# Kernel tuning notes

Measured on AMD Instinct MI355X. Metric: run time of the kernel, lower is better.

The kernel has to match this reference:

```python
import jax, jax.numpy as jnp
import numpy as np
import math

B, T, D, H, V, L = 8, 512, 128, 512, 50257, 8
DT = 1.0
RAW_INIT = math.log(math.expm1(1.0))  # so softplus(raw) == 1.0


def setup_inputs() -> dict:
    key = jax.random.key(0)
    ks = jax.random.split(key, 8)
    x = jax.random.randint(ks[0], (B, T), 0, V)
    E = jax.random.normal(ks[1], (V, D), jnp.float32) * 0.02
    P = jax.random.normal(ks[2], (T, D), jnp.float32) * 0.01
    W0 = jax.random.normal(ks[3], (2 * D, H), jnp.float32) * 0.02
    W1 = jax.random.normal(ks[4], (H, H), jnp.float32) * 0.02
    W2 = jax.random.normal(ks[5], (H, H), jnp.float32) * 0.02
    W3 = jax.random.normal(ks[6], (H, 1), jnp.float32) * 0.002
    return {
        'x': x, 'E': E, 'P': P,
        'W0': W0, 'b0': jnp.zeros((H,), jnp.float32),
        'W1': W1, 'b1': jnp.zeros((H,), jnp.float32),
        'W2': W2, 'b2': jnp.zeros((H,), jnp.float32),
        'W3': W3, 'b3': jnp.zeros((1,), jnp.float32),
        'raw_m_bias': jnp.asarray(RAW_INIT, jnp.float32),
        'raw_gamma': jnp.asarray(RAW_INIT, jnp.float32),
    }


def causal_cumulative_mean(h):
    t = h.shape[1]
    denom = jnp.arange(1, t + 1, dtype=h.dtype)[None, :, None]
    return jnp.cumsum(h, axis=1) / denom


def mlp_energy_sum(xi, h, W0, b0, W1, b1, W2, b2, W3, b3):
    z = jnp.concatenate([xi, h], axis=-1)  # (B,T,2D)
    z = jax.nn.gelu(z @ W0 + b0, approximate=False)
    z = jax.nn.gelu(z @ W1 + b1, approximate=False)
    z = jax.nn.gelu(z @ W2 + b2, approximate=False)
    return jnp.sum(z @ W3 + b3)


def reference(x, E, P, W0, b0, W1, b1, W2, b2, W3, b3, raw_m_bias, raw_gamma):
    emb = E[x] + P[None, :T]  # (B,T,D)
    gamma = jax.nn.softplus(raw_gamma)
    m = jax.nn.softplus(raw_m_bias) + 0.001  # global mass
    h = emb
    v = jnp.zeros_like(h)
    for _ in range(L):
        # causal_force=True: xi built from detached h
        xi = causal_cumulative_mean(jax.lax.stop_gradient(h))
        grad_V = jax.grad(
            lambda hh: mlp_energy_sum(xi, hh, W0, b0, W1, b1, W2, b2, W3, b3)
        )(h)
        f = -grad_V
        v = (v + DT * f / m) / (1.0 + DT * gamma)
        h = h + DT * v
    logits = jnp.einsum('btd,vd->btv', h, E)  # (B,T,V)
    return logits
```

## Files before the change

kernel.cpp:

```cpp
#include <hip/hip_runtime.h>
#include <hip/hip_bf16.h>

typedef __attribute__((ext_vector_type(8))) short short8;
typedef __attribute__((ext_vector_type(4))) float f32x4;

#define DEV static __device__ __forceinline__

DEV void gelu_pair(float x, float& z, float& dz){
  float ax = fabsf(x)*0.70710678118654752f;
  float e  = __expf(-ax*ax);
  float t  = __fdividef(1.0f, 1.0f + 0.3275911f*ax);
  float poly = t*(0.254829592f + t*(-0.284496736f + t*(1.421413741f +
               t*(-1.453152027f + t*1.061405429f))));
  float erfv = 1.0f - poly*e;
  erfv = x < 0.0f ? -erfv : erfv;
  float cdf = 0.5f*(1.0f + erfv);
  z  = x*cdf;
  dz = cdf + x*0.39894228040143268f*e;
}
DEV float dgelu_f(float x){ float zz, dz; gelu_pair(x, zz, dz); return dz; }
DEV float softplus_f(float x){ return log1pf(expf(x)); }
DEV void store_f4_a4(float* p, f32x4 v){ __builtin_memcpy(p, &v, 16); }

DEV void gload_lds16(const __hip_bfloat16* g, __hip_bfloat16* l){
  __builtin_amdgcn_global_load_lds((const __attribute__((address_space(1))) void*)g,
                                   (__attribute__((address_space(3))) void*)l, 16, 0, 0);
}

DEV unsigned pack2bf(float a, float b){
  __hip_bfloat16 ba = __float2bfloat16(a), bb = __float2bfloat16(b);
  unsigned short ua, ub;
  __builtin_memcpy(&ua, &ba, 2); __builtin_memcpy(&ub, &bb, 2);
  return (unsigned)ua | ((unsigned)ub << 16);
}
DEV float unp_lo(unsigned u){ union{unsigned x; float f;} c; c.x = u << 16; return c.f; }
DEV float unp_hi(unsigned u){ union{unsigned x; float f;} c; c.x = u & 0xffff0000u; return c.f; }

__global__ __launch_bounds__(512) void embed_k(const int* __restrict__ x,
                        const float* __restrict__ E, const float* __restrict__ P,
                        float* __restrict__ h, float* __restrict__ v,
                        float* __restrict__ S){
  int bid = blockIdx.x;
  int row = threadIdx.x >> 5;
  int q   = threadIdx.x & 31;
  int tok = bid*16 + row;
  int t   = tok & 511;
  int id  = x[tok];
  float4 e4 = ((const float4*)E)[(size_t)id*32 + q];
  float4 p4 = ((const float4*)P)[(size_t)t*32 + q];
  float4 val; val.x=e4.x+p4.x; val.y=e4.y+p4.y; val.z=e4.z+p4.z; val.w=e4.w+p4.w;
  float4 z4 = {0.f,0.f,0.f,0.f};
  ((float4*)h)[(size_t)tok*32 + q] = val;
  ((float4*)v)[(size_t)tok*32 + q] = z4;
  __shared__ float4 ps[16][32];
  ps[row][q] = val;
  __syncthreads();
  if (row==0){
    float4 s = ps[0][q];
    #pragma unroll
    for (int r=1;r<16;r++){
      float4 t4 = ps[r][q];
      s.x+=t4.x; s.y+=t4.y; s.z+=t4.z; s.w+=t4.w;
    }
    ((float4*)S)[(size_t)bid*32 + q] = s;
  }
}

__global__ void convw_k(const float* __restrict__ W0, const float* __restrict__ W1,
                        const float* __restrict__ W2,
                        __hip_bfloat16* __restrict__ W0T, __hip_bfloat16* __restrict__ W1T,
                        __hip_bfloat16* __restrict__ W2T, __hip_bfloat16* __restrict__ W2b,
                        __hip_bfloat16* __restrict__ W1b, __hip_bfloat16* __restrict__ W0h){
  int i = blockIdx.x*256 + threadIdx.x;
  if (i < 131072){
    int e=i&7, n=(i>>3)&511, kk=i>>12; int k=(kk>>2)*32+(kk&3)*8+e;
    W0T[i]=__float2bfloat16(W0[(size_t)k*512+n]);
  } else if (i < 393216){
    int j=i-131072; int e=j&7, n=(j>>3)&511, kk=j>>12; int k=(kk>>2)*32+(kk&3)*8+e;
    W1T[j]=__float2bfloat16(W1[(size_t)k*512+n]);
  } else if (i < 655360){
    int j=i-393216; int e=j&7, n=(j>>3)&511, kk=j>>12; int k=(kk>>2)*32+(kk&3)*8+e;
    W2T[j]=__float2bfloat16(W2[(size_t)k*512+n]);
  } else if (i < 917504){
    int j=i-655360; int e=j&7, n=(j>>3)&511, kk=j>>12; int k=(kk>>2)*32+(kk&3)*8+e;
    W2b[j]=__float2bfloat16(W2[(size_t)n*512+k]);
  } else if (i < 1179648){
    int j=i-917504; int e=j&7, n=(j>>3)&511, kk=j>>12; int k=(kk>>2)*32+(kk&3)*8+e;
    W1b[j]=__float2bfloat16(W1[(size_t)n*512+k]);
  } else if (i < 1245184){
    int j=i-1179648; int e=j&7, n=(j>>3)&127, kk=j>>10; int k=(kk>>2)*32+(kk&3)*8+e;
    W0h[j]=__float2bfloat16(W0[(size_t)(128+n)*512+k]);
  }
}
__global__ void conv_c4_k(const float* __restrict__ W, __hip_bfloat16* __restrict__ Wb, int n4){
  int i = blockIdx.x*256 + threadIdx.x;
  if (i < n4){
    float4 f = ((const float4*)W)[i];
    Wb[4*i+0]=__float2bfloat16(f.x);
    Wb[4*i+1]=__float2bfloat16(f.y);
    Wb[4*i+2]=__float2bfloat16(f.z);
    Wb[4*i+3]=__float2bfloat16(f.w);
  }
}

struct LayerP {
  const __hip_bfloat16 *W0T,*W1T,*W2T,*W2b,*W1b,*W0h;
  const float *b0,*b1,*b2,*W3;
  float *v, *h; __hip_bfloat16* hbf;
  const float* Sprev; float* Snext;
  const float *rawm,*rawg;
};

template<int KSTEPS, int NW, int NF>
DEV void wpre(const __hip_bfloat16* __restrict__ Wt, int nbase, int r16, int g,
              short8 (&bb)[6][NF]){
  const __hip_bfloat16* wp = Wt + ((size_t)g*NW + nbase + r16)*8;
  #pragma unroll
  for (int d=0; d<5; d++){
    if (d < KSTEPS){
      #pragma unroll
      for (int f=0; f<NF; f++)
        bb[d][f] = *(const short8*)&wp[((size_t)d*4*NW + (size_t)f*16)*8];
    }
  }
}

template<int KSTEPS, int NW, int NF>
DEV void gphase(const __hip_bfloat16* __restrict__ Wt,
                const __hip_bfloat16* __restrict__ zin,
                int nbase, int r16, int g, f32x4 (&acc)[NF],
                short8 (&bb)[6][NF]){
  #pragma unroll
  for (int f=0;f<NF;f++) acc[f] = (f32x4){0.f,0.f,0.f,0.f};
  const __hip_bfloat16* wp = Wt + ((size_t)g*NW + nbase + r16)*8;
  #pragma unroll
  for (int s=0; s<KSTEPS; s++){
    if (s+5 < KSTEPS){
      const __hip_bfloat16* wn = wp + (size_t)(s+5)*4*NW*8;
      #pragma unroll
      for (int f=0; f<NF; f++)
        bb[(s+5)%6][f] = *(const short8*)&wn[(size_t)f*128];
    }
    short8 a = *(const short8*)&zin[(s*4+g)*128 + r16*8];
    #pragma unroll
    for (int f=0; f<NF; f++)
      acc[f] = __builtin_amdgcn_mfma_f32_16x16x32_bf16(a, bb[s%6][f], acc[f],0,0,0);
  }
}

__global__ __launch_bounds__(1024,4) void layer_k(LayerP p){
  __shared__ __align__(16) __hip_bfloat16 sZ[2][8192];
  __shared__ float4 psum[16][32];
  const int tid = threadIdx.x;
  const int w = tid >> 6, lane = tid & 63;
  const int r16 = lane & 15, g = lane >> 4;
  const int rb = blockIdx.x;
  const int nb = w*32;

  short8 bb[6][2];

  if (tid < 512){
    const int row = tid >> 5;
    const int lane32 = tid & 31;
    const int b = rb >> 5, c = rb & 31;
    float4 pfx = {0.f,0.f,0.f,0.f};
    const float4* S4 = (const float4*)(p.Sprev + (size_t)b*32*128) + lane32;
    for (int cc=0; cc<c; cc++){
      float4 t = S4[(size_t)cc*32];
      pfx.x+=t.x; pfx.y+=t.y; pfx.z+=t.z; pfx.w+=t.w;
    }
    float4 myrow = ((const float4*)(p.h + (size_t)rb*16*128))[(size_t)row*32 + lane32];
    psum[row][lane32] = myrow;
    __syncthreads();
    for (int rr=0; rr<row; rr++){
      float4 t = psum[rr][lane32];
      pfx.x+=t.x; pfx.y+=t.y; pfx.z+=t.z; pfx.w+=t.w;
    }
    pfx.x+=myrow.x; pfx.y+=myrow.y; pfx.z+=myrow.z; pfx.w+=myrow.w;
    float inv = 1.0f/(float)(c*16 + row + 1);
    const int d0 = lane32*4;
    union { ushort4 v; __hip_bfloat16 e[4]; } ux, uh;
    ux.e[0]=__float2bfloat16(pfx.x*inv); ux.e[1]=__float2bfloat16(pfx.y*inv);
    ux.e[2]=__float2bfloat16(pfx.z*inv); ux.e[3]=__float2bfloat16(pfx.w*inv);
    uh.e[0]=__float2bfloat16(myrow.x); uh.e[1]=__float2bfloat16(myrow.y);
    uh.e[2]=__float2bfloat16(myrow.z); uh.e[3]=__float2bfloat16(myrow.w);
    *(ushort4*)&sZ[0][(d0>>3)*128      + row*8 + (d0&7)] = ux.v;
    *(ushort4*)&sZ[0][(16+(d0>>3))*128 + row*8 + (d0&7)] = uh.v;
  } else {
    __syncthreads();
  }
  wpre<8,512,2>(p.W0T, nb, r16, g, bb);
  __syncthreads();

  f32x4 acc[2];
  unsigned g1p[2][2], g2p[2][2];

  gphase<8,512,2>(p.W0T, sZ[0], nb, r16, g, acc, bb);
  wpre<16,512,2>(p.W1T, nb, r16, g, bb);
  #pragma unroll
  for (int f=0; f<2; f++){
    int n = nb + f*16 + r16;
    float bias = p.b0[n];
    #pragma unroll
    for (int jp=0; jp<2; jp++){
      float z0, dz0, z1v, dz1;
      gelu_pair(acc[f][2*jp]   + bias, z0,  dz0);
      gelu_pair(acc[f][2*jp+1] + bias, z1v, dz1);
      g1p[f][jp] = pack2bf(dz0, dz1);
      sZ[1][(n>>3)*128 + (g*4+2*jp)*8   + (n&7)] = __float2bfloat16(z0);
      sZ[1][(n>>3)*128 + (g*4+2*jp+1)*8 + (n&7)] = __float2bfloat16(z1v);
    }
  }
  __syncthreads();

  gphase<16,512,2>(p.W1T, sZ[1], nb, r16, g, acc, bb);
  wpre<16,512,2>(p.W2T, nb, r16, g, bb);
  #pragma unroll
  for (int f=0; f<2; f++){
    int n = nb + f*16 + r16;
    float bias = p.b1[n];
    #pragma unroll
    for (int jp=0; jp<2; jp++){
      float z0, dz0, z1v, dz1;
      gelu_pair(acc[f][2*jp]   + bias, z0,  dz0);
      gelu_pair(acc[f][2*jp+1] + bias, z1v, dz1);
      g2p[f][jp] = pack2bf(dz0, dz1);
      sZ[0][(n>>3)*128 + (g*4+2*jp)*8   + (n&7)] = __float2bfloat16(z0);
      sZ[0][(n>>3)*128 + (g*4+2*jp+1)*8 + (n&7)] = __float2bfloat16(z1v);
    }
  }
  __syncthreads();

  gphase<16,512,2>(p.W2T, sZ[0], nb, r16, g, acc, bb);
  wpre<16,512,2>(p.W2b, nb, r16, g, bb);
  #pragma unroll
  for (int f=0; f<2; f++){
    int n = nb + f*16 + r16;
    float bias = p.b2[n];
    float w3 = p.W3[n];
    #pragma unroll
    for (int j=0;j<4;j++){
      float xx = acc[f][j] + bias;
      sZ[1][(n>>3)*128 + (g*4+j)*8 + (n&7)] = __float2bfloat16(w3*dgelu_f(xx));
    }
  }
  __syncthreads();

  gphase<16,512,2>(p.W2b, sZ[1], nb, r16, g, acc, bb);
  wpre<16,512,2>(p.W1b, nb, r16, g, bb);
  #pragma unroll
  for (int f=0; f<2; f++){
    int n = nb + f*16 + r16;
    #pragma unroll
    for (int jp=0; jp<2; jp++){
      float gv0 = unp_lo(g2p[f][jp]), gv1 = unp_hi(g2p[f][jp]);
      sZ[0][(n>>3)*128 + (g*4+2*jp)*8   + (n&7)] = __float2bfloat16(acc[f][2*jp]*gv0);
      sZ[0][(n>>3)*128 + (g*4+2*jp+1)*8 + (n&7)] = __float2bfloat16(acc[f][2*jp+1]*gv1);
    }
  }
  __syncthreads();

  gphase<16,512,2>(p.W1b, sZ[0], nb, r16, g, acc, bb);
  short8 bbF[6][1];
  if (w < 8) wpre<16,128,1>(p.W0h, w*16, r16, g, bbF);
  #pragma unroll
  for (int f=0; f<2; f++){
    int n = nb + f*16 + r16;
    #pragma unroll
    for (int jp=0; jp<2; jp++){
      float gv0 = unp_lo(g1p[f][jp]), gv1 = unp_hi(g1p[f][jp]);
      sZ[1][(n>>3)*128 + (g*4+2*jp)*8   + (n&7)] = __float2bfloat16(acc[f][2*jp]*gv0);
      sZ[1][(n>>3)*128 + (g*4+2*jp+1)*8 + (n&7)] = __float2bfloat16(acc[f][2*jp+1]*gv1);
    }
  }
  __syncthreads();

  if (w < 8){
    f32x4 accF[1];
    gphase<16,128,1>(p.W0h, sZ[1], w*16, r16, g, accF, bbF);
    float im  = 1.0f/(softplus_f(p.rawm[0]) + 0.001f);
    float fac = 1.0f/(1.0f + softplus_f(p.rawg[0]));
    int col = w*16 + r16;
    float hs = 0.f;
    #pragma unroll
    for (int j=0;j<4;j++){
      int row = g*4 + j;
      size_t o = ((size_t)rb*16 + row)*128 + col;
      float nv = (p.v[o] - accF[0][j]*im)*fac;
      p.v[o] = nv;
      float nh = p.h[o] + nv;
      p.h[o] = nh;
      p.hbf[o] = __float2bfloat16(nh);
      hs += nh;
    }
    hs += __shfl_xor(hs, 16);
    hs += __shfl_xor(hs, 32);
    if (g==0) p.Snext[(size_t)rb*128 + col] = hs;
  }
}

__global__ __launch_bounds__(256,4) void logits_k(const __hip_bfloat16* __restrict__ A,
                                                  const __hip_bfloat16* __restrict__ Bt,
                                                  float* __restrict__ out){
  constexpr int V = 50257;
  __shared__ __align__(16) __hip_bfloat16 sA[128*64];
  __shared__ __align__(16) __hip_bfloat16 sB[128*64];
  const int tid = threadIdx.x, lane = tid & 63, wave = tid >> 6;
  const int wg = ((blockIdx.x & 7) * 1572) + (blockIdx.x >> 3);
  const int mt = wg & 31, nt = wg >> 5;
  const int m0 = mt*128, n0 = nt*128;
  const int wm = (wave>>1)*64, wn = (wave&1)*64;
  const int r16 = lane & 15, g = lane >> 4;
  const int srow = tid >> 3;
  const int scol = ((tid & 7) ^ (srow & 7)) * 8;
  const int sx = (r16 & 7) * 8;
  f32x4 zero = {0.f,0.f,0.f,0.f};
  f32x4 acc[4][4];
  #pragma unroll
  for (int i=0;i<4;i++){ acc[i][0]=zero; acc[i][1]=zero; acc[i][2]=zero; acc[i][3]=zero; }

  auto stageA = [&](int ks){
    #pragma unroll
    for (int i=0;i<4;i++)
      gload_lds16(A + (size_t)(m0 + i*32 + srow)*128 + ks*64 + scol,
                  &sA[i*2048 + wave*512]);
  };
  auto stageB = [&](int ks){
    #pragma unroll
    for (int i=0;i<4;i++){
      int r = n0 + i*32 + srow; if (r > V-1) r = V-1;
      gload_lds16(Bt + (size_t)r*128 + ks*64 + scol,
                  &sB[i*2048 + wave*512]);
    }
  };
  stageA(0); stageB(0);
  __syncthreads();
  #pragma unroll
  for (int ks=0; ks<2; ks++){
    #pragma unroll
    for (int kk=0; kk<2; kk++){
      const int ko = kk*32 + g*8;
      short8 a[4], b[4];
      #pragma unroll
      for (int ti=0; ti<4; ti++) a[ti] = *(const short8*)&sA[(wm + ti*16 + r16)*64 + (ko ^ sx)];
      #pragma unroll
      for (int tj=0; tj<4; tj++) b[tj] = *(const short8*)&sB[(wn + tj*16 + r16)*64 + (ko ^ sx)];
      #pragma unroll
      for (int tb=0; tb<4; tb++)
        #pragma unroll
        for (int ta=0; ta<4; ta++)
          acc[tb][ta] = __builtin_amdgcn_mfma_f32_16x16x32_bf16(b[tb],a[ta],acc[tb][ta],0,0,0);
    }
    if (ks==0){
      __syncthreads();
      stageA(1); stageB(1);
      __syncthreads();
    }
  }
  #pragma unroll
  for (int tb=0; tb<4; tb++){
    #pragma unroll
    for (int ta=0; ta<4; ta++){
      int row = m0 + wm + ta*16 + r16;
      int n   = n0 + wn + tb*16 + g*4;
      f32x4 c = acc[tb][ta];
      float* po = out + (size_t)row*V + n;
      if (n + 3 < V){
        store_f4_a4(po, c);
      } else {
        #pragma unroll
        for (int j=0;j<4;j++) if (n+j < V) po[j] = c[j];
      }
    }
  }
}

extern "C" void kernel_launch(void* const* d_in, const int* in_sizes, int n_in,
                              void* d_out, int out_size, void* d_ws, size_t ws_size,
                              hipStream_t stream){
  const int*   x    = (const int*)  d_in[0];
  const float* E    = (const float*)d_in[1];
  const float* P    = (const float*)d_in[2];
  const float* W0   = (const float*)d_in[3];
  const float* b0   = (const float*)d_in[4];
  const float* W1   = (const float*)d_in[5];
  const float* b1   = (const float*)d_in[6];
  const float* W2   = (const float*)d_in[7];
  const float* b2   = (const float*)d_in[8];
  const float* W3   = (const float*)d_in[9];
  const float* rawm = (const float*)d_in[11];
  const float* rawg = (const float*)d_in[12];

  constexpr int B=8, T=512, D=128, H=512, V=50257, L=8;
  const int M = B*T;

  char* w = (char*)d_ws;
  auto alloc = [&](size_t bytes)->char*{ char* r = w; w += (bytes + 255) & ~(size_t)255; return r; };
  float* h            = (float*)alloc((size_t)M*D*4);
  float* v            = (float*)alloc((size_t)M*D*4);
  __hip_bfloat16* hbf = (__hip_bfloat16*)alloc((size_t)M*D*2);
  float* S0           = (float*)alloc((size_t)B*32*128*4);
  float* S1           = (float*)alloc((size_t)B*32*128*4);
  __hip_bfloat16* W0T = (__hip_bfloat16*)alloc((size_t)131072*2);
  __hip_bfloat16* W1T = (__hip_bfloat16*)alloc((size_t)262144*2);
  __hip_bfloat16* W2T = (__hip_bfloat16*)alloc((size_t)262144*2);
  __hip_bfloat16* W2b = (__hip_bfloat16*)alloc((size_t)262144*2);
  __hip_bfloat16* W1b = (__hip_bfloat16*)alloc((size_t)262144*2);
  __hip_bfloat16* W0h = (__hip_bfloat16*)alloc((size_t)65536*2);
  __hip_bfloat16* Ebf = (__hip_bfloat16*)alloc((size_t)V*D*2);

  convw_k  <<<4864, 256, 0, stream>>>(W0, W1, W2, W0T, W1T, W2T, W2b, W1b, W0h);
  conv_c4_k<<<(V*D/4+255)/256, 256, 0, stream>>>(E, Ebf, V*D/4);
  embed_k<<<M/16, 512, 0, stream>>>(x, E, P, h, v, S0);

  LayerP lp{};
  lp.W0T=W0T; lp.W1T=W1T; lp.W2T=W2T; lp.W2b=W2b; lp.W1b=W1b; lp.W0h=W0h;
  lp.b0=b0; lp.b1=b1; lp.b2=b2; lp.W3=W3;
  lp.v=v; lp.h=h; lp.hbf=hbf; lp.rawm=rawm; lp.rawg=rawg;

  for (int l=0; l<L; l++){
    lp.Sprev = (l&1) ? S1 : S0;
    lp.Snext = (l&1) ? S0 : S1;
    layer_k<<<M/16, 1024, 0, stream>>>(lp);
  }
  logits_k<<<12576, 256, 0, stream>>>(hbf, Ebf, (float*)d_out);
}
```

Measured before the change: 591.3 us.

## Parallelize chunk prefix sum, prefetch h/v early, skip redundant layer stores

The serial per-thread loop over previous chunk sums becomes a parallel partial sum across rows, reduced through a second shared buffer, and the in-chunk prefix loop becomes a fixed-length predicated unrolled loop. The h and v loads and the softplus scalars are hoisted to the kernel start, and the W0 weight prefetch is issued before the prefix phase so that latency overlaps. The first layer treats v as zero instead of reading it, and embed no longer zeroes v. Only the last layer writes hbf, and it skips the h, v and chunk-sum writes. Holding the prefetched values costs extra registers at 1024 threads per block.

After: 570.5 us. -3.5%, faster.

```diff
diff --git a/kernel.cpp b/kernel.cpp
--- a/kernel.cpp
+++ b/kernel.cpp
@@ -38,8 +38,7 @@
 
 __global__ __launch_bounds__(512) void embed_k(const int* __restrict__ x,
                         const float* __restrict__ E, const float* __restrict__ P,
-                        float* __restrict__ h, float* __restrict__ v,
-                        float* __restrict__ S){
+                        float* __restrict__ h, float* __restrict__ S){
   int bid = blockIdx.x;
   int row = threadIdx.x >> 5;
   int q   = threadIdx.x & 31;
@@ -49,9 +48,7 @@
   float4 e4 = ((const float4*)E)[(size_t)id*32 + q];
   float4 p4 = ((const float4*)P)[(size_t)t*32 + q];
   float4 val; val.x=e4.x+p4.x; val.y=e4.y+p4.y; val.z=e4.z+p4.z; val.w=e4.w+p4.w;
-  float4 z4 = {0.f,0.f,0.f,0.f};
   ((float4*)h)[(size_t)tok*32 + q] = val;
-  ((float4*)v)[(size_t)tok*32 + q] = z4;
   __shared__ float4 ps[16][32];
   ps[row][q] = val;
   __syncthreads();
@@ -109,6 +106,7 @@
   float *v, *h; __hip_bfloat16* hbf;
   const float* Sprev; float* Snext;
   const float *rawm,*rawg;
+  int first, last;
 };
 
 template<int KSTEPS, int NW, int NF>
@@ -151,6 +149,7 @@
 __global__ __launch_bounds__(1024,4) void layer_k(LayerP p){
   __shared__ __align__(16) __hip_bfloat16 sZ[2][8192];
   __shared__ float4 psum[16][32];
+  __shared__ float4 psumC[16][32];
   const int tid = threadIdx.x;
   const int w = tid >> 6, lane = tid & 63;
   const int r16 = lane & 15, g = lane >> 4;
@@ -159,22 +158,50 @@
 
   short8 bb[6][2];
 
+  wpre<8,512,2>(p.W0T, nb, r16, g, bb);
+  float vr[4] = {0.f,0.f,0.f,0.f}, hr[4] = {0.f,0.f,0.f,0.f};
+  float im = 0.f, fac = 0.f;
+  if (w < 8){
+    const int col = w*16 + r16;
+    #pragma unroll
+    for (int j=0;j<4;j++){
+      size_t o = ((size_t)rb*16 + g*4 + j)*128 + col;
+      hr[j] = p.h[o];
+      vr[j] = p.first ? 0.f : p.v[o];
+    }
+    im  = 1.0f/(softplus_f(p.rawm[0]) + 0.001f);
+    fac = 1.0f/(1.0f + softplus_f(p.rawg[0]));
+  }
+
   if (tid < 512){
     const int row = tid >> 5;
     const int lane32 = tid & 31;
     const int b = rb >> 5, c = rb & 31;
+    const float4* S4 = (const float4*)(p.Sprev + (size_t)b*32*128) + lane32;
+    float4 part = {0.f,0.f,0.f,0.f};
+    if (row < c){
+      float4 t = S4[(size_t)row*32];
+      part.x+=t.x; part.y+=t.y; part.z+=t.z; part.w+=t.w;
+    }
+    if (row+16 < c){
+      float4 t = S4[(size_t)(row+16)*32];
+      part.x+=t.x; part.y+=t.y; part.z+=t.z; part.w+=t.w;
+    }
+    float4 myrow = ((const float4*)(p.h + (size_t)rb*16*128))[(size_t)row*32 + lane32];
+    psum[row][lane32]  = myrow;
+    psumC[row][lane32] = part;
+    __syncthreads();
     float4 pfx = {0.f,0.f,0.f,0.f};
-    const float4* S4 = (const float4*)(p.Sprev + (size_t)b*32*128) + lane32;
-    for (int cc=0; cc<c; cc++){
-      float4 t = S4[(size_t)cc*32];
+    #pragma unroll
+    for (int r=0;r<16;r++){
+      float4 t = psumC[r][lane32];
       pfx.x+=t.x; pfx.y+=t.y; pfx.z+=t.z; pfx.w+=t.w;
     }
-    float4 myrow = ((const float4*)(p.h + (size_t)rb*16*128))[(size_t)row*32 + lane32];
-    psum[row][lane32] = myrow;
-    __syncthreads();
-    for (int rr=0; rr<row; rr++){
+    #pragma unroll
+    for (int rr=0; rr<15; rr++){
       float4 t = psum[rr][lane32];
-      pfx.x+=t.x; pfx.y+=t.y; pfx.z+=t.z; pfx.w+=t.w;
+      float sel = rr < row ? 1.0f : 0.0f;
+      pfx.x += sel*t.x; pfx.y += sel*t.y; pfx.z += sel*t.z; pfx.w += sel*t.w;
     }
     pfx.x+=myrow.x; pfx.y+=myrow.y; pfx.z+=myrow.z; pfx.w+=myrow.w;
     float inv = 1.0f/(float)(c*16 + row + 1);
@@ -189,7 +216,6 @@
   } else {
     __syncthreads();
   }
-  wpre<8,512,2>(p.W0T, nb, r16, g, bb);
   __syncthreads();
 
   f32x4 acc[2];
@@ -278,24 +304,23 @@
   if (w < 8){
     f32x4 accF[1];
     gphase<16,128,1>(p.W0h, sZ[1], w*16, r16, g, accF, bbF);
-    float im  = 1.0f/(softplus_f(p.rawm[0]) + 0.001f);
-    float fac = 1.0f/(1.0f + softplus_f(p.rawg[0]));
     int col = w*16 + r16;
     float hs = 0.f;
     #pragma unroll
     for (int j=0;j<4;j++){
       int row = g*4 + j;
       size_t o = ((size_t)rb*16 + row)*128 + col;
-      float nv = (p.v[o] - accF[0][j]*im)*fac;
-      p.v[o] = nv;
-      float nh = p.h[o] + nv;
-      p.h[o] = nh;
-      p.hbf[o] = __float2bfloat16(nh);
+      float nv = (vr[j] - accF[0][j]*im)*fac;
+      float nh = hr[j] + nv;
+      if (!p.last){ p.v[o] = nv; p.h[o] = nh; }
+      else        { p.hbf[o] = __float2bfloat16(nh); }
       hs += nh;
     }
-    hs += __shfl_xor(hs, 16);
-    hs += __shfl_xor(hs, 32);
-    if (g==0) p.Snext[(size_t)rb*128 + col] = hs;
+    if (!p.last){
+      hs += __shfl_xor(hs, 16);
+      hs += __shfl_xor(hs, 32);
+      if (g==0) p.Snext[(size_t)rb*128 + col] = hs;
+    }
   }
 }
 
@@ -411,7 +436,7 @@
 
   convw_k  <<<4864, 256, 0, stream>>>(W0, W1, W2, W0T, W1T, W2T, W2b, W1b, W0h);
   conv_c4_k<<<(V*D/4+255)/256, 256, 0, stream>>>(E, Ebf, V*D/4);
-  embed_k<<<M/16, 512, 0, stream>>>(x, E, P, h, v, S0);
+  embed_k<<<M/16, 512, 0, stream>>>(x, E, P, h, S0);
 
   LayerP lp{};
   lp.W0T=W0T; lp.W1T=W1T; lp.W2T=W2T; lp.W2b=W2b; lp.W1b=W1b; lp.W0h=W0h;
@@ -421,6 +446,8 @@
   for (int l=0; l<L; l++){
     lp.Sprev = (l&1) ? S1 : S0;
     lp.Snext = (l&1) ? S0 : S1;
+    lp.first = (l==0) ? 1 : 0;
+    lp.last  = (l==L-1) ? 1 : 0;
     layer_k<<<M/16, 1024, 0, stream>>>(lp);
   }
   logits_k<<<12576, 256, 0, stream>>>(hbf, Ebf, (float*)d_out);
```
